# Performance work log

Hardware: AMD Instinct MI355X
Metric: run time of the kernel (lower is better)

The kernel has to match this reference:

```python
import jax, jax.numpy as jnp
import numpy as np

N = 20000
E = 160000
H = 8          # heads
D = 96         # head_dim (768 // 8)
C = H * D      # 768 hidden channels
G = 256        # num graphs
NUM_CLASSES = 32
SLOPE = 0.2    # GATv2 LeakyReLU negative slope


def layer_norm(x, w, b, eps=1e-5):
    mu = jnp.mean(x, axis=-1, keepdims=True)
    var = jnp.mean(jnp.square(x - mu), axis=-1, keepdims=True)
    return (x - mu) * jax.lax.rsqrt(var + eps) * w + b


def gatv2_layer(x, src, dst, Wl, bl, Wr, br, att, bias):
    # x: [N, C]; src/dst: [E'] with self loops included
    xl = (x @ Wl + bl).reshape(N, H, D)   # source projection
    xr = (x @ Wr + br).reshape(N, H, D)   # target projection
    e = xl[src] + xr[dst]                 # [E', H, D] edge gather
    e = jnp.where(e > 0, e, SLOPE * e)    # LeakyReLU
    logits = jnp.einsum('ehd,hd->eh', e, att)  # [E', H]
    m = jax.ops.segment_max(logits, dst, num_segments=N)
    ex = jnp.exp(logits - m[dst])
    s = jax.ops.segment_sum(ex, dst, num_segments=N)
    alpha = ex / s[dst]                   # segment softmax over in-edges
    out = jax.ops.segment_sum(alpha[:, :, None] * xl[src], dst, num_segments=N)
    return out.reshape(N, C) + bias


def setup_inputs() -> dict:
    key = jax.random.key(0)
    ks = jax.random.split(key, 24)
    x = jax.random.normal(ks[0], (N, 768), jnp.float32)
    edge_index = jax.random.randint(ks[1], (2, E), 0, N, jnp.int64)
    batch = jnp.sort(jax.random.randint(ks[2], (N,), 0, G, jnp.int64))
    sc = 1.0 / np.sqrt(C)
    p = {
        'x': x, 'edge_index': edge_index, 'batch': batch,
        'w_in': jax.random.normal(ks[3], (768, C), jnp.float32) * sc,
        'b_in': jnp.zeros((C,), jnp.float32),
        'Wl': jax.random.normal(ks[4], (3, C, C), jnp.float32) * sc,
        'bl': jnp.zeros((3, C), jnp.float32),
        'Wr': jax.random.normal(ks[5], (3, C, C), jnp.float32) * sc,
        'br': jnp.zeros((3, C), jnp.float32),
        'att': jax.random.normal(ks[6], (3, H, D), jnp.float32) * (1.0 / np.sqrt(D)),
        'gat_bias': jnp.zeros((3, C), jnp.float32),
        'ln_w': jnp.ones((3, C), jnp.float32),
        'ln_b': jnp.zeros((3, C), jnp.float32),
        'out_ln_w': jnp.ones((3 * C,), jnp.float32),
        'out_ln_b': jnp.zeros((3 * C,), jnp.float32),
        'w_out': jax.random.normal(ks[7], (3 * C, NUM_CLASSES), jnp.float32) * (1.0 / np.sqrt(3 * C)),
        'b_out': jnp.zeros((NUM_CLASSES,), jnp.float32),
    }
    return p


def reference(x, edge_index, batch, w_in, b_in, Wl, bl, Wr, br, att, gat_bias,
              ln_w, ln_b, out_ln_w, out_ln_b, w_out, b_out):
    # add self loops (PyG add_self_loops=True)
    loops = jnp.arange(N, dtype=edge_index.dtype)
    src = jnp.concatenate([edge_index[0], loops])
    dst = jnp.concatenate([edge_index[1], loops])

    h = x @ w_in + b_in
    jumps = []
    for l in range(3):
        a = gatv2_layer(h, src, dst, Wl[l], bl[l], Wr[l], br[l], att[l], gat_bias[l])
        h = layer_norm(a + h, ln_w[l], ln_b[l])
        h = jax.nn.gelu(h, approximate=False)
        jumps.append(h)
    hc = jnp.concatenate(jumps, axis=-1)  # JumpingKnowledge 'cat' -> [N, 3C]

    # global mean pool over graphs
    sums = jax.ops.segment_sum(hc, batch, num_segments=G)
    cnt = jax.ops.segment_sum(jnp.ones((N, 1), hc.dtype), batch, num_segments=G)
    pooled = sums / jnp.maximum(cnt, 1.0)

    out = layer_norm(pooled, out_ln_w, out_ln_b)
    return out @ w_out + b_out
```

## Files before the change

kernel.cpp:

```cpp
#include <hip/hip_runtime.h>

#define N_NODES 20000
#define N_EDGES 160000
#define CH      768
#define CH3     2304
#define NGRAPH  256
#define NCLS    32

typedef __bf16 bf16v8 __attribute__((ext_vector_type(8)));
typedef float  f32x4  __attribute__((ext_vector_type(4)));

__device__ __forceinline__ float b2f(ushort u) {
    union { float f; unsigned u; } x; x.u = ((unsigned)u) << 16; return x.f;
}
__device__ __forceinline__ ushort f2b(float f) {
    union { float f; unsigned u; } x; x.f = f;
    unsigned r = x.u + 0x7FFFu + ((x.u >> 16) & 1u);
    return (ushort)(r >> 16);
}
__device__ __forceinline__ void load12(const ushort* __restrict__ p, float* o) {
    const ushort4* q = (const ushort4*)p;
    ushort4 a = q[0], b = q[1], c = q[2];
    o[0]=b2f(a.x); o[1]=b2f(a.y); o[2]=b2f(a.z); o[3]=b2f(a.w);
    o[4]=b2f(b.x); o[5]=b2f(b.y); o[6]=b2f(b.z); o[7]=b2f(b.w);
    o[8]=b2f(c.x); o[9]=b2f(c.y); o[10]=b2f(c.z); o[11]=b2f(c.w);
}
__device__ __forceinline__ void load12f(const float* __restrict__ p, float* o) {
    const float4* q = (const float4*)p;
    float4 a = q[0], b = q[1], c = q[2];
    o[0]=a.x; o[1]=a.y; o[2]=a.z; o[3]=a.w;
    o[4]=b.x; o[5]=b.y; o[6]=b.z; o[7]=b.w;
    o[8]=c.x; o[9]=c.y; o[10]=c.z; o[11]=c.w;
}
__device__ __forceinline__ void async_copy16(void* lds, const void* gp) {
    __builtin_amdgcn_global_load_lds((const void __attribute__((address_space(1)))*)gp,
                                     (void __attribute__((address_space(3)))*)lds, 16, 0, 0);
}

__global__ void cvt_x_kernel(const float* __restrict__ src, ushort* __restrict__ dst, int n4) {
    int i = blockIdx.x * 256 + threadIdx.x;
    if (i >= n4) return;
    float4 v = ((const float4*)src)[i];
    ushort4 o; o.x = f2b(v.x); o.y = f2b(v.y); o.z = f2b(v.z); o.w = f2b(v.w);
    ((ushort4*)dst)[i] = o;
}

__global__ void transpose_cvt_all(const float* __restrict__ w_in,
                                  const float* __restrict__ Wl,
                                  const float* __restrict__ Wr,
                                  ushort* __restrict__ wt_in,
                                  ushort* __restrict__ wt_l) {
    __shared__ float tile[32][33];
    int z = blockIdx.z;
    const float* in;
    ushort* out;
    if (z == 0) { in = w_in; out = wt_in; }
    else {
        int l = (z - 1) >> 1, isr = (z - 1) & 1;
        in  = (isr ? Wr : Wl) + (size_t)l * CH * CH;
        out = wt_l + (size_t)l * 1536 * CH + (size_t)isr * CH * CH;
    }
    int bx = blockIdx.x * 32, by = blockIdx.y * 32;
    int tx = threadIdx.x, ty = threadIdx.y;
    #pragma unroll
    for (int i = ty; i < 32; i += 8) tile[i][tx] = in[(size_t)(by + i) * CH + bx + tx];
    __syncthreads();
    #pragma unroll
    for (int i = ty; i < 32; i += 8) out[(size_t)(bx + i) * CH + by + tx] = f2b(tile[tx][i]);
}

__global__ void count_both_kernel(const int* __restrict__ dst, int* __restrict__ deg, int e,
                                  const int* __restrict__ batch, int* __restrict__ gcount, int n) {
    int i = blockIdx.x * 256 + threadIdx.x;
    if (i < e) atomicAdd(&deg[dst[i]], 1);
    if (i < n) { atomicAdd(&deg[i], 1); atomicAdd(&gcount[batch[i]], 1); }
}
__global__ __launch_bounds__(1024) void scan_kernel(const int* __restrict__ deg,
                                                    int* __restrict__ rowptr, int n) {
    __shared__ int part[1024];
    int t = threadIdx.x;
    const int chunk = (n + 1023) / 1024;
    int base = t * chunk;
    int s = 0;
    for (int i = 0; i < chunk; ++i) { int idx = base + i; if (idx < n) s += deg[idx]; }
    part[t] = s; __syncthreads();
    for (int off = 1; off < 1024; off <<= 1) {
        int v = (t >= off) ? part[t - off] : 0;
        __syncthreads();
        part[t] += v;
        __syncthreads();
    }
    int run = (t == 0) ? 0 : part[t - 1];
    for (int i = 0; i < chunk; ++i) {
        int idx = base + i;
        if (idx < n) { rowptr[idx] = run; run += deg[idx]; }
    }
    if (t == 1023) rowptr[n] = part[1023];
}
__global__ void selfloop_kernel(const int* __restrict__ rowptr, int* __restrict__ csrc,
                                int* __restrict__ cursor, int n) {
    int i = blockIdx.x * 256 + threadIdx.x;
    if (i < n) { int p = rowptr[i]; csrc[p] = i; cursor[i] = p + 1; }
}
__global__ void scatter_kernel(const int* __restrict__ src, const int* __restrict__ dst,
                               int* __restrict__ cursor, int* __restrict__ csrc, int e) {
    int i = blockIdx.x * 256 + threadIdx.x;
    if (i < e) { int p = atomicAdd(&cursor[dst[i]], 1); csrc[p] = src[i]; }
}
__global__ __launch_bounds__(256) void gscan_kernel(const int* __restrict__ gcount,
                                                    int* __restrict__ gstart) {
    __shared__ int p[256];
    int t = threadIdx.x;
    p[t] = gcount[t]; __syncthreads();
    for (int off = 1; off < 256; off <<= 1) {
        int v = (t >= off) ? p[t - off] : 0;
        __syncthreads();
        p[t] += v;
        __syncthreads();
    }
    gstart[t] = p[t] - gcount[t];
    if (t == 255) gstart[256] = p[255];
}

__global__ __launch_bounds__(512, 2) void gemm8_bf16_kernel(
    const ushort* __restrict__ A, int lda,
    const ushort* __restrict__ Bt,
    const float* __restrict__ biasA, const float* __restrict__ biasB, int nsplit,
    ushort* __restrict__ C, int ldc, int M, int ncolt) {
    __shared__ __bf16 As[4][256 * 32];
    __shared__ __bf16 Bs[4][256 * 32];
    int tid = threadIdx.x;
    int wid = tid >> 6, lane = tid & 63;
    int wm = wid >> 2, wn = wid & 3;
    int l16 = lane & 15, lq = lane >> 4;

    int nwg = gridDim.x, bid = blockIdx.x;
    int q = nwg >> 3, rm = nwg & 7;
    int xcd = bid & 7, idx = bid >> 3;
    int wg = (xcd < rm ? xcd * (q + 1) : rm * (q + 1) + (xcd - rm) * q) + idx;
    int row_t = wg / ncolt, col_t = wg - row_t * ncolt;
    int row0 = row_t * 256, col0 = col_t * 256;

    int s1 = 512 + tid;
    int r0 = tid >> 2, r1 = s1 >> 2;
    int ac0 = ((tid & 3) ^ ((tid >> 3) & 3)) * 8;
    int ac1 = ((s1 & 3) ^ ((s1 >> 3) & 3)) * 8;
    const ushort* pa0 = A + (size_t)min(row0 + r0, M - 1) * lda + ac0;
    const ushort* pa1 = A + (size_t)min(row0 + r1, M - 1) * lda + ac1;
    const ushort* pb0 = Bt + (size_t)(col0 + r0) * CH + ac0;
    const ushort* pb1 = Bt + (size_t)(col0 + r1) * CH + ac1;
    int wb0 = (wid * 64) * 8, wb1 = (512 + wid * 64) * 8;

    int koffE = (lq ^ ((l16 >> 1) & 3)) * 8;

    f32x4 acc[8][4] = {};

    #define STAGE_A(buf, t) do { int k0 = (t) * 32;                   \
        async_copy16(&As[buf][wb0], pa0 + k0);                        \
        async_copy16(&As[buf][wb1], pa1 + k0); } while (0)
    #define STAGE_B(buf, t) do { int k0 = (t) * 32;                   \
        async_copy16(&Bs[buf][wb0], pb0 + k0);                        \
        async_copy16(&Bs[buf][wb1], pb1 + k0); } while (0)

    STAGE_A(0, 0); STAGE_B(0, 0);
    STAGE_A(1, 1); STAGE_B(1, 1);
    STAGE_A(2, 2); STAGE_B(2, 2);
    asm volatile("s_waitcnt vmcnt(8)" ::: "memory");
    __builtin_amdgcn_s_barrier();

    for (int t = 0; t < 24; ++t) {
        int buf = t & 3, sbuf = (t + 3) & 3;
        const __bf16* Ab = &As[buf][(wm * 128 + l16) * 32 + koffE];
        const __bf16* Bb = &Bs[buf][(wn * 64 + l16) * 32 + koffE];
        bf16v8 av[4], bv[4];
        #pragma unroll
        for (int f = 0; f < 4; ++f) av[f] = *(const bf16v8*)(Ab + f * 16 * 32);
        #pragma unroll
        for (int g = 0; g < 4; ++g) bv[g] = *(const bf16v8*)(Bb + g * 16 * 32);
        if (t < 21) STAGE_A(sbuf, t + 3);
        __builtin_amdgcn_s_barrier();
        asm volatile("s_waitcnt lgkmcnt(0)" ::: "memory");
        __builtin_amdgcn_sched_barrier(0);
        __builtin_amdgcn_s_setprio(1);
        #pragma unroll
        for (int f = 0; f < 4; ++f)
            #pragma unroll
            for (int g = 0; g < 4; ++g)
                acc[f][g] = __builtin_amdgcn_mfma_f32_16x16x32_bf16(av[f], bv[g], acc[f][g], 0, 0, 0);
        __builtin_amdgcn_s_setprio(0);
        __builtin_amdgcn_s_barrier();
        #pragma unroll
        for (int f = 0; f < 4; ++f) av[f] = *(const bf16v8*)(Ab + (64 + f * 16) * 32);
        if (t < 21) STAGE_B(sbuf, t + 3);
        __builtin_amdgcn_s_barrier();
        asm volatile("s_waitcnt lgkmcnt(0)" ::: "memory");
        __builtin_amdgcn_sched_barrier(0);
        __builtin_amdgcn_s_setprio(1);
        #pragma unroll
        for (int f = 0; f < 4; ++f)
            #pragma unroll
            for (int g = 0; g < 4; ++g)
                acc[4 + f][g] = __builtin_amdgcn_mfma_f32_16x16x32_bf16(av[f], bv[g], acc[4 + f][g], 0, 0, 0);
        __builtin_amdgcn_s_setprio(0);
        if (t < 21)       { asm volatile("s_waitcnt vmcnt(8)" ::: "memory"); }
        else if (t == 21) { asm volatile("s_waitcnt vmcnt(4)" ::: "memory"); }
        else if (t == 22) { asm volatile("s_waitcnt vmcnt(0)" ::: "memory"); }
        __builtin_amdgcn_s_barrier();
    }
    #undef STAGE_A
    #undef STAGE_B

    float bias[4];
    #pragma unroll
    for (int g = 0; g < 4; ++g) {
        int col = col0 + wn * 64 + g * 16 + l16;
        bias[g] = (col < nsplit) ? biasA[col] : biasB[col - nsplit];
    }
    #pragma unroll
    for (int f = 0; f < 8; ++f) {
        int mbase = row0 + wm * 128 + f * 16 + lq * 4;
        #pragma unroll
        for (int g = 0; g < 4; ++g) {
            int col = col0 + wn * 64 + g * 16 + l16;
            #pragma unroll
            for (int r = 0; r < 4; ++r) {
                int mm = mbase + r;
                if (mm < M) C[(size_t)mm * ldc + col] = f2b(acc[f][g][r] + bias[g]);
            }
        }
    }
}

__global__ __launch_bounds__(256) void gat_node_kernel(
    const ushort* __restrict__ xlxr,
    const ushort* __restrict__ hin, int ldh,
    const int* __restrict__ rowptr, const int* __restrict__ csrc,
    const float* __restrict__ att, const float* __restrict__ gbias,
    const float* __restrict__ lnw, const float* __restrict__ lnb,
    ushort* __restrict__ hout, int nn) {
    int wv = threadIdx.x >> 6, lane = threadIdx.x & 63;
    int n = blockIdx.x * 4 + wv;
    int c0 = lane * 12;
    const ushort* __restrict__ xbase = xlxr + c0;
    float attv[12], xr[12], acc1[12] = {}, acc2[12] = {};
    load12f(att + c0, attv);
    load12(xbase + (size_t)n * 1536 + CH, xr);
    float s1 = 0.f, s2 = 0.f;
    int rs = rowptr[n], re = rowptr[n + 1];
    int e = rs;
    for (; e + 1 < re; e += 2) {
        int sa = csrc[e], sb = csrc[e + 1];
        float xa[12], xb[12];
        load12(xbase + (size_t)sa * 1536, xa);
        load12(xbase + (size_t)sb * 1536, xb);
        float da = 0.f, db = 0.f;
        #pragma unroll
        for (int j = 0; j < 12; ++j) {
            float va = xa[j] + xr[j]; va = fmaxf(va, 0.2f * va);
            float vb = xb[j] + xr[j]; vb = fmaxf(vb, 0.2f * vb);
            da = fmaf(va, attv[j], da);
            db = fmaf(vb, attv[j], db);
        }
        da += __shfl_xor(da, 1); db += __shfl_xor(db, 1);
        da += __shfl_xor(da, 2); db += __shfl_xor(db, 2);
        da += __shfl_xor(da, 4); db += __shfl_xor(db, 4);
        float ea = __expf(da), eb = __expf(db);
        s1 += ea; s2 += eb;
        #pragma unroll
        for (int j = 0; j < 12; ++j) {
            acc1[j] = fmaf(ea, xa[j], acc1[j]);
            acc2[j] = fmaf(eb, xb[j], acc2[j]);
        }
    }
    if (e < re) {
        int sa = csrc[e];
        float xa[12];
        load12(xbase + (size_t)sa * 1536, xa);
        float da = 0.f;
        #pragma unroll
        for (int j = 0; j < 12; ++j) {
            float va = xa[j] + xr[j]; va = fmaxf(va, 0.2f * va);
            da = fmaf(va, attv[j], da);
        }
        da += __shfl_xor(da, 1);
        da += __shfl_xor(da, 2);
        da += __shfl_xor(da, 4);
        float ea = __expf(da);
        s1 += ea;
        #pragma unroll
        for (int j = 0; j < 12; ++j) acc1[j] = fmaf(ea, xa[j], acc1[j]);
    }
    float inv = 1.f / (s1 + s2);
    float hres[12], gb[12], tv[12];
    load12(hin + (size_t)n * ldh + c0, hres);
    load12f(gbias + c0, gb);
    float lsum = 0.f, lsq = 0.f;
    #pragma unroll
    for (int j = 0; j < 12; ++j) {
        tv[j] = (acc1[j] + acc2[j]) * inv + gb[j] + hres[j];
        lsum += tv[j];
        lsq = fmaf(tv[j], tv[j], lsq);
    }
    #pragma unroll
    for (int o = 1; o < 64; o <<= 1) { lsum += __shfl_xor(lsum, o); lsq += __shfl_xor(lsq, o); }
    float mu = lsum * (1.f / 768.f);
    float var = lsq * (1.f / 768.f) - mu * mu;
    float rstd = rsqrtf(var + 1e-5f);
    float wv12[12], bv12[12];
    load12f(lnw + c0, wv12);
    load12f(lnb + c0, bv12);
    ushort* op = hout + (size_t)n * CH3 + c0;
    ushort4 u[3];
    #pragma unroll
    for (int k = 0; k < 3; ++k) {
        float g[4];
        #pragma unroll
        for (int q = 0; q < 4; ++q) {
            int j = k * 4 + q;
            float y = (tv[j] - mu) * rstd * wv12[j] + bv12[j];
            g[q] = 0.5f * y * (1.f + erff(y * 0.70710678118f));
        }
        u[k].x = f2b(g[0]); u[k].y = f2b(g[1]); u[k].z = f2b(g[2]); u[k].w = f2b(g[3]);
        ((ushort4*)op)[k] = u[k];
    }
}

__global__ __launch_bounds__(256) void pool_kernel(const ushort* __restrict__ hc,
                                                   const int* __restrict__ gstart,
                                                   float* __restrict__ pooled) {
    int g = blockIdx.x;
    int c = blockIdx.y * 256 + threadIdx.x;
    int s = gstart[g], e = gstart[g + 1];
    const ushort* p = hc + (size_t)s * CH3 + c;
    float a0 = 0.f, a1 = 0.f, a2 = 0.f, a3 = 0.f;
    int n = s;
    for (; n + 3 < e; n += 4) {
        a0 += b2f(p[0]);
        a1 += b2f(p[CH3]);
        a2 += b2f(p[2 * CH3]);
        a3 += b2f(p[3 * CH3]);
        p += 4 * CH3;
    }
    for (; n < e; ++n) { a0 += b2f(*p); p += CH3; }
    float a = (a0 + a1) + (a2 + a3);
    pooled[(size_t)g * CH3 + c] = a * (1.f / (float)max(e - s, 1));
}

__global__ __launch_bounds__(256) void head_kernel(const float* __restrict__ pooled,
                                                   const float* __restrict__ olnw,
                                                   const float* __restrict__ olnb,
                                                   const float* __restrict__ wout,
                                                   const float* __restrict__ bout,
                                                   float* __restrict__ outp) {
    __shared__ float row[CH3];
    __shared__ float red[8];
    __shared__ float parts[8][32];
    int g = blockIdx.x, t = threadIdx.x;
    int lane = t & 63, wv = t >> 6;
    float s = 0.f;
    for (int c = t; c < CH3; c += 256) { float v = pooled[(size_t)g * CH3 + c]; row[c] = v; s += v; }
    #pragma unroll
    for (int o = 1; o < 64; o <<= 1) s += __shfl_xor(s, o);
    if (lane == 0) red[wv] = s;
    __syncthreads();
    float mu = (red[0] + red[1] + red[2] + red[3]) * (1.f / (float)CH3);
    float q = 0.f;
    for (int c = t; c < CH3; c += 256) { float d = row[c] - mu; q += d * d; }
    #pragma unroll
    for (int o = 1; o < 64; o <<= 1) q += __shfl_xor(q, o);
    if (lane == 0) red[4 + wv] = q;
    __syncthreads();
    float rstd = rsqrtf((red[4] + red[5] + red[6] + red[7]) * (1.f / (float)CH3) + 1e-5f);
    for (int c = t; c < CH3; c += 256)
        row[c] = (row[c] - mu) * rstd * olnw[c] + olnb[c];
    __syncthreads();
    int j = t & 31, slice = t >> 5;
    float a = 0.f;
    int cb = slice * (CH3 / 8);
    for (int c = cb; c < cb + CH3 / 8; ++c) a += row[c] * wout[(size_t)c * 32 + j];
    parts[slice][j] = a;
    __syncthreads();
    if (t < 32) {
        float r = bout[t];
        #pragma unroll
        for (int si = 0; si < 8; ++si) r += parts[si][t];
        outp[(size_t)g * 32 + t] = r;
    }
}

extern "C" void kernel_launch(void* const* d_in, const int* in_sizes, int n_in,
                              void* d_out, int out_size, void* d_ws, size_t ws_size,
                              hipStream_t stream) {
    const float* x     = (const float*)d_in[0];
    const int*   ei    = (const int*)d_in[1];
    const int*   batch = (const int*)d_in[2];
    const float* w_in  = (const float*)d_in[3];
    const float* b_in  = (const float*)d_in[4];
    const float* Wl    = (const float*)d_in[5];
    const float* bl    = (const float*)d_in[6];
    const float* Wr    = (const float*)d_in[7];
    const float* br    = (const float*)d_in[8];
    const float* att   = (const float*)d_in[9];
    const float* gbias = (const float*)d_in[10];
    const float* lnw   = (const float*)d_in[11];
    const float* lnb   = (const float*)d_in[12];
    const float* olnw  = (const float*)d_in[13];
    const float* olnb  = (const float*)d_in[14];
    const float* wout  = (const float*)d_in[15];
    const float* bout  = (const float*)d_in[16];

    char* ws = (char*)d_ws;
    size_t off = 0;
    auto alloc = [&](size_t bytes) -> void* {
        void* p = ws + off;
        off = (off + bytes + 255) & ~(size_t)255;
        return p;
    };
    ushort* h0     = (ushort*)alloc((size_t)N_NODES * CH * 2);
    ushort* hc     = (ushort*)alloc((size_t)N_NODES * CH3 * 2);
    ushort* xlxr   = (ushort*)alloc((size_t)N_NODES * 1536 * 2);
    ushort* wt_in  = (ushort*)alloc((size_t)CH * CH * 2);
    ushort* wt_l   = (ushort*)alloc((size_t)3 * 1536 * CH * 2);
    int*    deg    = (int*)alloc((size_t)N_NODES * 4);
    int*    rowptr = (int*)alloc((size_t)(N_NODES + 1) * 4);
    int*    cursor = (int*)alloc((size_t)N_NODES * 4);
    int*    csrc   = (int*)alloc((size_t)(N_EDGES + N_NODES) * 4);
    int*    gcount = (int*)alloc(256 * 4);
    int*    gstart = (int*)alloc(257 * 4);
    float*  pooled = (float*)alloc((size_t)NGRAPH * CH3 * 4);
    if (off > ws_size) return;

    ushort* xc = hc;

    cvt_x_kernel<<<(N_NODES * CH / 4 + 255) / 256, 256, 0, stream>>>(x, xc, N_NODES * CH / 4);
    transpose_cvt_all<<<dim3(24, 24, 7), dim3(32, 8), 0, stream>>>(w_in, Wl, Wr, wt_in, wt_l);

    int nb = (N_NODES + 255) / 256, eb = (N_EDGES + 255) / 256;
    hipMemsetAsync(deg, 0, (size_t)N_NODES * 4, stream);
    hipMemsetAsync(gcount, 0, 256 * 4, stream);
    count_both_kernel<<<eb, 256, 0, stream>>>(ei + N_EDGES, deg, N_EDGES, batch, gcount, N_NODES);
    scan_kernel<<<1, 1024, 0, stream>>>(deg, rowptr, N_NODES);
    selfloop_kernel<<<nb, 256, 0, stream>>>(rowptr, csrc, cursor, N_NODES);
    scatter_kernel<<<eb, 256, 0, stream>>>(ei, ei + N_EDGES, cursor, csrc, N_EDGES);
    gscan_kernel<<<1, 256, 0, stream>>>(gcount, gstart);

    gemm8_bf16_kernel<<<79 * 3, 512, 0, stream>>>(
        xc, CH, wt_in, b_in, b_in, CH, h0, CH, N_NODES, 3);

    for (int l = 0; l < 3; ++l) {
        const ushort* hprev = (l == 0) ? h0 : (hc + (size_t)(l - 1) * CH);
        int ldh = (l == 0) ? CH : CH3;
        gemm8_bf16_kernel<<<79 * 6, 512, 0, stream>>>(
            hprev, ldh, wt_l + (size_t)l * 1536 * CH,
            bl + (size_t)l * CH, br + (size_t)l * CH, CH,
            xlxr, 1536, N_NODES, 6);
        gat_node_kernel<<<N_NODES / 4, 256, 0, stream>>>(
            xlxr, hprev, ldh, rowptr, csrc,
            att + (size_t)l * CH, gbias + (size_t)l * CH,
            lnw + (size_t)l * CH, lnb + (size_t)l * CH,
            hc + (size_t)l * CH, N_NODES);
    }

    pool_kernel<<<dim3(NGRAPH, CH3 / 256), 256, 0, stream>>>(hc, gstart, pooled);
    head_kernel<<<NGRAPH, 256, 0, stream>>>(pooled, olnw, olnb, wout, bout, (float*)d_out);
}
```

Before: 725.4 us.

## Restructure bf16 GEMM to double-buffered 64-wide K tiles

Replaces the 4-stage, 32-wide K pipeline in the bf16 projection GEMM with a 2-stage double buffer of 64-wide K tiles. Each iteration does twice the MFMA work per barrier, and the split A/B staging with interleaved barriers becomes a single prefetch followed by one full vmcnt(0) wait. The goal is to cut barrier and synchronisation overhead per unit of work and widen the LDS swizzle to 8 chunks. In exchange the prefetch depth drops to one tile, which may expose global load latency, and the vector registers needed for operands double.

```diff
diff --git a/kernel.cpp b/kernel.cpp
--- a/kernel.cpp
+++ b/kernel.cpp
@@ -127,8 +127,8 @@
     const ushort* __restrict__ Bt,
     const float* __restrict__ biasA, const float* __restrict__ biasB, int nsplit,
     ushort* __restrict__ C, int ldc, int M, int ncolt) {
-    __shared__ __bf16 As[4][256 * 32];
-    __shared__ __bf16 Bs[4][256 * 32];
+    __shared__ __align__(16) __bf16 As[2][256 * 64];
+    __shared__ __align__(16) __bf16 Bs[2][256 * 64];
     int tid = threadIdx.x;
     int wid = tid >> 6, lane = tid & 63;
     int wm = wid >> 2, wn = wid & 3;
@@ -141,74 +141,84 @@
     int row_t = wg / ncolt, col_t = wg - row_t * ncolt;
     int row0 = row_t * 256, col0 = col_t * 256;
 
-    int s1 = 512 + tid;
-    int r0 = tid >> 2, r1 = s1 >> 2;
-    int ac0 = ((tid & 3) ^ ((tid >> 3) & 3)) * 8;
-    int ac1 = ((s1 & 3) ^ ((s1 >> 3) & 3)) * 8;
-    const ushort* pa0 = A + (size_t)min(row0 + r0, M - 1) * lda + ac0;
-    const ushort* pa1 = A + (size_t)min(row0 + r1, M - 1) * lda + ac1;
-    const ushort* pb0 = Bt + (size_t)(col0 + r0) * CH + ac0;
-    const ushort* pb1 = Bt + (size_t)(col0 + r1) * CH + ac1;
-    int wb0 = (wid * 64) * 8, wb1 = (512 + wid * 64) * 8;
-
-    int koffE = (lq ^ ((l16 >> 1) & 3)) * 8;
+    int ak = (((tid & 7) ^ ((tid >> 3) & 7)) << 3);
+    const ushort* gA[4];
+    const ushort* gB[4];
+    #pragma unroll
+    for (int r = 0; r < 4; ++r) {
+        int ra = min(row0 + r * 64 + (tid >> 3), M - 1);
+        gA[r] = A + (size_t)ra * lda + ak;
+        gB[r] = Bt + (size_t)(col0 + r * 64 + (tid >> 3)) * CH + ak;
+    }
+    int ldst = wid << 9;
+
+    int swz = l16 & 7;
+    int arow = wm * 128 + l16;
+    int brow = wn * 64 + l16;
+    int kc0 = ((lq ^ swz) << 3);
+    int kc1 = (((4 + lq) ^ swz) << 3);
 
     f32x4 acc[8][4] = {};
 
-    #define STAGE_A(buf, t) do { int k0 = (t) * 32;                   \
-        async_copy16(&As[buf][wb0], pa0 + k0);                        \
-        async_copy16(&As[buf][wb1], pa1 + k0); } while (0)
-    #define STAGE_B(buf, t) do { int k0 = (t) * 32;                   \
-        async_copy16(&Bs[buf][wb0], pb0 + k0);                        \
-        async_copy16(&Bs[buf][wb1], pb1 + k0); } while (0)
-
-    STAGE_A(0, 0); STAGE_B(0, 0);
-    STAGE_A(1, 1); STAGE_B(1, 1);
-    STAGE_A(2, 2); STAGE_B(2, 2);
-    asm volatile("s_waitcnt vmcnt(8)" ::: "memory");
+    #define STAGE(buf, kof) do { _Pragma("unroll")                         \
+        for (int r = 0; r < 4; ++r) {                                      \
+            async_copy16(&As[buf][(r << 12) + ldst], gA[r] + (kof));       \
+            async_copy16(&Bs[buf][(r << 12) + ldst], gB[r] + (kof));       \
+        } } while (0)
+
+    STAGE(0, 0);
+    asm volatile("s_waitcnt vmcnt(0)" ::: "memory");
     __builtin_amdgcn_s_barrier();
-
-    for (int t = 0; t < 24; ++t) {
-        int buf = t & 3, sbuf = (t + 3) & 3;
-        const __bf16* Ab = &As[buf][(wm * 128 + l16) * 32 + koffE];
-        const __bf16* Bb = &Bs[buf][(wn * 64 + l16) * 32 + koffE];
-        bf16v8 av[4], bv[4];
-        #pragma unroll
-        for (int f = 0; f < 4; ++f) av[f] = *(const bf16v8*)(Ab + f * 16 * 32);
-        #pragma unroll
-        for (int g = 0; g < 4; ++g) bv[g] = *(const bf16v8*)(Bb + g * 16 * 32);
-        if (t < 21) STAGE_A(sbuf, t + 3);
-        __builtin_amdgcn_s_barrier();
-        asm volatile("s_waitcnt lgkmcnt(0)" ::: "memory");
+    __builtin_amdgcn_sched_barrier(0);
+
+    for (int t = 0; t < 12; ++t) {
+        int buf = t & 1;
+        if (t < 11) STAGE(buf ^ 1, (t + 1) * 64);
         __builtin_amdgcn_sched_barrier(0);
+        const __bf16* Ab = &As[buf][arow * 64];
+        const __bf16* Bb = &Bs[buf][brow * 64];
+        bf16v8 a0[4], a1[4], b0[4], b1[4];
+        #pragma unroll
+        for (int g = 0; g < 4; ++g) {
+            b0[g] = *(const bf16v8*)(Bb + g * 16 * 64 + kc0);
+            b1[g] = *(const bf16v8*)(Bb + g * 16 * 64 + kc1);
+        }
+        #pragma unroll
+        for (int f = 0; f < 4; ++f) {
+            a0[f] = *(const bf16v8*)(Ab + f * 16 * 64 + kc0);
+            a1[f] = *(const bf16v8*)(Ab + f * 16 * 64 + kc1);
+        }
         __builtin_amdgcn_s_setprio(1);
         #pragma unroll
         for (int f = 0; f < 4; ++f)
             #pragma unroll
-            for (int g = 0; g < 4; ++g)
-                acc[f][g] = __builtin_amdgcn_mfma_f32_16x16x32_bf16(av[f], bv[g], acc[f][g], 0, 0, 0);
+            for (int g = 0; g < 4; ++g) {
+                acc[f][g] = __builtin_amdgcn_mfma_f32_16x16x32_bf16(a0[f], b0[g], acc[f][g], 0, 0, 0);
+                acc[f][g] = __builtin_amdgcn_mfma_f32_16x16x32_bf16(a1[f], b1[g], acc[f][g], 0, 0, 0);
+            }
         __builtin_amdgcn_s_setprio(0);
-        __builtin_amdgcn_s_barrier();
-        #pragma unroll
-        for (int f = 0; f < 4; ++f) av[f] = *(const bf16v8*)(Ab + (64 + f * 16) * 32);
-        if (t < 21) STAGE_B(sbuf, t + 3);
-        __builtin_amdgcn_s_barrier();
-        asm volatile("s_waitcnt lgkmcnt(0)" ::: "memory");
-        __builtin_amdgcn_sched_barrier(0);
+        #pragma unroll
+        for (int f = 0; f < 4; ++f) {
+            a0[f] = *(const bf16v8*)(Ab + (64 + f * 16) * 64 + kc0);
+            a1[f] = *(const bf16v8*)(Ab + (64 + f * 16) * 64 + kc1);
+        }
         __builtin_amdgcn_s_setprio(1);
         #pragma unroll
         for (int f = 0; f < 4; ++f)
             #pragma unroll
-            for (int g = 0; g < 4; ++g)
-                acc[4 + f][g] = __builtin_amdgcn_mfma_f32_16x16x32_bf16(av[f], bv[g], acc[4 + f][g], 0, 0, 0);
+            for (int g = 0; g < 4; ++g) {
+                acc[4 + f][g] = __builtin_amdgcn_mfma_f32_16x16x32_bf16(a0[f], b0[g], acc[4 + f][g], 0, 0, 0);
+                acc[4 + f][g] = __builtin_amdgcn_mfma_f32_16x16x32_bf16(a1[f], b1[g], acc[4 + f][g], 0, 0, 0);
+            }
         __builtin_amdgcn_s_setprio(0);
-        if (t < 21)       { asm volatile("s_waitcnt vmcnt(8)" ::: "memory"); }
-        else if (t == 21) { asm volatile("s_waitcnt vmcnt(4)" ::: "memory"); }
-        else if (t == 22) { asm volatile("s_waitcnt vmcnt(0)" ::: "memory"); }
-        __builtin_amdgcn_s_barrier();
-    }
-    #undef STAGE_A
-    #undef STAGE_B
+        if (t < 11) {
+            __builtin_amdgcn_sched_barrier(0);
+            asm volatile("s_waitcnt vmcnt(0)" ::: "memory");
+            __builtin_amdgcn_s_barrier();
+            __builtin_amdgcn_sched_barrier(0);
+        }
+    }
+    #undef STAGE
 
     float bias[4];
     #pragma unroll
```

Measured after the change: 673.1 us. 7.2% less time.
